# Kernel optimization log

Measured on AMD Instinct MI355X. Metric: run time of the kernel, lower is better.

The kernel has to match this reference:

```python
import jax, jax.numpy as jnp
import numpy as np

HEADS = 64
DIM_HEAD = 64
SCALE = DIM_HEAD ** -0.5
EPS = 1e-6


def setup_inputs() -> dict:
    key = jax.random.key(0)
    ks = jax.random.split(key, 6)
    b, s, dim = 2, 4096, 1024
    inner = HEADS * DIM_HEAD  # 4096
    std = 0.02
    return {
        "x": jax.random.normal(ks[0], (b, s, dim), dtype=jnp.float32),
        "Wq": jax.random.normal(ks[1], (dim, inner), dtype=jnp.float32) * std,
        "Wk": jax.random.normal(ks[2], (dim, inner), dtype=jnp.float32) * std,
        "Wv": jax.random.normal(ks[3], (dim, inner), dtype=jnp.float32) * std,
        "Wo": jax.random.normal(ks[4], (inner, dim), dtype=jnp.float32) * std,
        "bo": jnp.zeros((dim,), dtype=jnp.float32),
    }


def reference(x, Wq, Wk, Wv, Wo, bo):
    b, s, dim = x.shape
    h, dh = HEADS, DIM_HEAD
    # projections -> [b, s, h, dh]
    q = (x @ Wq).reshape(b, s, h, dh)
    k = (x @ Wk).reshape(b, s, h, dh)
    v = (x @ Wv).reshape(b, s, h, dh)
    # kernel feature map (relu) + scale on q
    q = jax.nn.relu(q) * SCALE
    k = jax.nn.relu(k)
    # NOTE: faithful to the source, these einsums contract over the HEAD axis
    # per token (i, j index heads; d indexes dim_head).
    kv = jnp.einsum('bsid,bsjd->bsdj', k, v)          # [b, s, dh, h]
    out = jnp.einsum('bsid,bsdj->bsij', q, kv)        # [b, s, h, h]
    q_norm = jnp.einsum('bsid,bsd->bsi', q, k.sum(axis=2))  # [b, s, h]
    out = out / (q_norm[..., None] + EPS)
    out = out.reshape(b, s, h * h)                    # h*h == h*dh since h == dh
    return out @ Wo + bo
```

## Files before the change

### kernel.cpp

```cpp
#include <hip/hip_runtime.h>
#include <hip/hip_bf16.h>
#include <cstdint>

#define M_TOK 8192
#define DIM   1024
#define INNER 4096
#define HEADS 64
#define DH    64
#define QSCALE 0.125f
#define EPS    1e-6f

typedef __hip_bfloat16 bf16;
typedef __bf16 bf16x8_t __attribute__((ext_vector_type(8)));
typedef float f32x4_t __attribute__((ext_vector_type(4)));

__device__ __forceinline__ float bfbits2f(unsigned short u) {
  return __uint_as_float(((unsigned)u) << 16);
}
__device__ __forceinline__ unsigned short f2bfbits(float f) {
  __hip_bfloat16 h = __float2bfloat16(f);
  unsigned short u;
  __builtin_memcpy(&u, &h, 2);
  return u;
}

__device__ __forceinline__ void load_lds16(const void* g, void* l) {
  __builtin_amdgcn_global_load_lds(
      (__attribute__((address_space(1))) void*)g,
      (__attribute__((address_space(3))) void*)l, 16, 0, 0);
}

__device__ __forceinline__ void asm_barrier() {
  asm volatile("s_barrier" ::: "memory");
}

__device__ __forceinline__ void swizzle_xy(int& bx, int& by) {
  const int gx = gridDim.x, gy = gridDim.y;
  const int id  = blockIdx.x + gx * blockIdx.y;
  const int per = gy >> 3;
  const int xcd = id & 7;
  const int s   = id >> 3;
  by = xcd * per + (s % per);
  bx = s / per;
}

__global__ __launch_bounds__(256) void castx_kernel(
    const float* __restrict__ x, unsigned short* __restrict__ xb, int n4)
{
  const int i = blockIdx.x * 256 + threadIdx.x;
  if (i < n4) {
    const float4 v = reinterpret_cast<const float4*>(x)[i];
    ushort4 o;
    o.x = f2bfbits(v.x); o.y = f2bfbits(v.y);
    o.z = f2bfbits(v.z); o.w = f2bfbits(v.w);
    reinterpret_cast<ushort4*>(xb)[i] = o;
  }
}

__global__ __launch_bounds__(256) void tcast_kernel(
    const float* __restrict__ W, unsigned short* __restrict__ Wt, int R, int C)
{
  __shared__ float tile[32][33];
  const int bx = blockIdx.x * 32;
  const int by = blockIdx.y * 32;
  const int tx = threadIdx.x & 31;
  const int ty = threadIdx.x >> 5;
#pragma unroll
  for (int k = 0; k < 4; ++k)
    tile[ty + k * 8][tx] = W[(size_t)(by + ty + k * 8) * C + bx + tx];
  __syncthreads();
#pragma unroll
  for (int k = 0; k < 4; ++k)
    Wt[(size_t)(bx + ty + k * 8) * R + by + tx] = f2bfbits(tile[tx][ty + k * 8]);
}

__global__ __launch_bounds__(256) void tcast_dual_kernel(
    const float* __restrict__ W0, const float* __restrict__ W1,
    unsigned short* __restrict__ Wt, int R, int C)
{
  __shared__ float tile[32][33];
  const float* W = blockIdx.z ? W1 : W0;
  unsigned short* dst = Wt + (size_t)blockIdx.z * R * C;
  const int bx = blockIdx.x * 32;
  const int by = blockIdx.y * 32;
  const int tx = threadIdx.x & 31;
  const int ty = threadIdx.x >> 5;
#pragma unroll
  for (int k = 0; k < 4; ++k)
    tile[ty + k * 8][tx] = W[(size_t)(by + ty + k * 8) * C + bx + tx];
  __syncthreads();
#pragma unroll
  for (int k = 0; k < 4; ++k)
    dst[(size_t)(bx + ty + k * 8) * R + by + tx] = f2bfbits(tile[tx][ty + k * 8]);
}

__device__ __forceinline__ void stage_half(
    const unsigned short* __restrict__ G, unsigned short* L,
    int rowbase, int k0, int K, int h, int tid)
{
#pragma unroll
  for (int j = 0; j < 2; ++j) {
    const int q  = h * 1024 + j * 512 + tid;
    const int r  = q >> 3;
    const int cg = (tid & 7) ^ (r & 7);
    load_lds16(&G[(size_t)(rowbase + r) * K + k0 + cg * 8], &L[q * 8]);
  }
}

template <int MODE, int DUAL>
__global__ __launch_bounds__(512, 2) void gemm256(
    const unsigned short* __restrict__ A,
    const unsigned short* __restrict__ Bt,
    unsigned short* __restrict__ C0,
    unsigned short* __restrict__ C1,
    int N, int K)
{
  __shared__ __align__(16) unsigned short As[2][256 * 64];
  __shared__ __align__(16) unsigned short Bs[2][256 * 64];

  int bxi, byi;
  swizzle_xy(bxi, byi);
  const int tid  = threadIdx.x;
  const int bm   = byi * 256;
  const int bn   = bxi * 256;
  const int lane = tid & 63;
  const int w    = tid >> 6;
  const int wm   = (w >> 2) * 128;
  const int wn   = (w & 3) * 64;
  const int quad = lane >> 4;
  const int l15  = lane & 15;

  f32x4_t acc[8][4];
#pragma unroll
  for (int mt = 0; mt < 8; ++mt)
#pragma unroll
    for (int nt = 0; nt < 4; ++nt) acc[mt][nt] = (f32x4_t){0.f, 0.f, 0.f, 0.f};

  const int NT = K >> 6;

  stage_half(A,  As[0], bm, 0,  K, 0, tid);
  stage_half(A,  As[0], bm, 0,  K, 1, tid);
  stage_half(Bt, Bs[0], bn, 0,  K, 0, tid);
  stage_half(Bt, Bs[0], bn, 0,  K, 1, tid);
  stage_half(A,  As[1], bm, 64, K, 0, tid);
  stage_half(A,  As[1], bm, 64, K, 1, tid);
  asm volatile("s_waitcnt vmcnt(4)" ::: "memory");
  asm_barrier();

  bf16x8_t af[8][2], bfr[4][2];

  for (int T = 0; T < NT; ++T) {
    const int c = T & 1;
    const unsigned short* Ac = As[c];
    const unsigned short* Bc = Bs[c];
    unsigned short* Bnx = Bs[c ^ 1];
    unsigned short* Anx = As[c];
    const int kB = (T + 1) * 64;
    const int kA = (T + 2) * 64;
    const bool pB = (T + 1 < NT);
    const bool pA = (T + 2 < NT);

#pragma unroll
    for (int mt = 0; mt < 4; ++mt) {
      const int r = wm + mt * 16 + l15;
#pragma unroll
      for (int kt = 0; kt < 2; ++kt) {
        const int s = (kt * 4 + quad) ^ (r & 7);
        af[mt][kt] = *reinterpret_cast<const bf16x8_t*>(&Ac[r * 64 + s * 8]);
      }
    }
#pragma unroll
    for (int nt = 0; nt < 2; ++nt) {
      const int r = wn + nt * 16 + l15;
#pragma unroll
      for (int kt = 0; kt < 2; ++kt) {
        const int s = (kt * 4 + quad) ^ (r & 7);
        bfr[nt][kt] = *reinterpret_cast<const bf16x8_t*>(&Bc[r * 64 + s * 8]);
      }
    }
    if (pB) stage_half(Bt, Bnx, bn, kB, K, 0, tid);
    asm_barrier();
    __builtin_amdgcn_s_setprio(1);
#pragma unroll
    for (int mt = 0; mt < 4; ++mt)
#pragma unroll
      for (int nt = 0; nt < 2; ++nt) {
        acc[mt][nt] = __builtin_amdgcn_mfma_f32_16x16x32_bf16(
            af[mt][0], bfr[nt][0], acc[mt][nt], 0, 0, 0);
        acc[mt][nt] = __builtin_amdgcn_mfma_f32_16x16x32_bf16(
            af[mt][1], bfr[nt][1], acc[mt][nt], 0, 0, 0);
      }
    __builtin_amdgcn_s_setprio(0);
    asm_barrier();

#pragma unroll
    for (int mt = 4; mt < 8; ++mt) {
      const int r = wm + mt * 16 + l15;
#pragma unroll
      for (int kt = 0; kt < 2; ++kt) {
        const int s = (kt * 4 + quad) ^ (r & 7);
        af[mt][kt] = *reinterpret_cast<const bf16x8_t*>(&Ac[r * 64 + s * 8]);
      }
    }
    if (pB) stage_half(Bt, Bnx, bn, kB, K, 1, tid);
    asm_barrier();
    __builtin_amdgcn_s_setprio(1);
#pragma unroll
    for (int mt = 4; mt < 8; ++mt)
#pragma unroll
      for (int nt = 0; nt < 2; ++nt) {
        acc[mt][nt] = __builtin_amdgcn_mfma_f32_16x16x32_bf16(
            af[mt][0], bfr[nt][0], acc[mt][nt], 0, 0, 0);
        acc[mt][nt] = __builtin_amdgcn_mfma_f32_16x16x32_bf16(
            af[mt][1], bfr[nt][1], acc[mt][nt], 0, 0, 0);
      }
    __builtin_amdgcn_s_setprio(0);
    asm_barrier();

#pragma unroll
    for (int nt = 2; nt < 4; ++nt) {
      const int r = wn + nt * 16 + l15;
#pragma unroll
      for (int kt = 0; kt < 2; ++kt) {
        const int s = (kt * 4 + quad) ^ (r & 7);
        bfr[nt][kt] = *reinterpret_cast<const bf16x8_t*>(&Bc[r * 64 + s * 8]);
      }
    }
    if (pA) stage_half(A, Anx, bm, kA, K, 0, tid);
    asm_barrier();
    __builtin_amdgcn_s_setprio(1);
#pragma unroll
    for (int mt = 0; mt < 4; ++mt)
#pragma unroll
      for (int nt = 2; nt < 4; ++nt) {
        acc[mt][nt] = __builtin_amdgcn_mfma_f32_16x16x32_bf16(
            af[mt][0], bfr[nt][0], acc[mt][nt], 0, 0, 0);
        acc[mt][nt] = __builtin_amdgcn_mfma_f32_16x16x32_bf16(
            af[mt][1], bfr[nt][1], acc[mt][nt], 0, 0, 0);
      }
    __builtin_amdgcn_s_setprio(0);
    asm_barrier();

    if (pA) stage_half(A, Anx, bm, kA, K, 1, tid);
    asm_barrier();
    __builtin_amdgcn_s_setprio(1);
#pragma unroll
    for (int mt = 4; mt < 8; ++mt)
#pragma unroll
      for (int nt = 2; nt < 4; ++nt) {
        acc[mt][nt] = __builtin_amdgcn_mfma_f32_16x16x32_bf16(
            af[mt][0], bfr[nt][0], acc[mt][nt], 0, 0, 0);
        acc[mt][nt] = __builtin_amdgcn_mfma_f32_16x16x32_bf16(
            af[mt][1], bfr[nt][1], acc[mt][nt], 0, 0, 0);
      }
    __builtin_amdgcn_s_setprio(0);
    if (T < NT - 2) {
      asm volatile("s_waitcnt vmcnt(4)" ::: "memory");
    } else {
      asm volatile("s_waitcnt vmcnt(0)" ::: "memory");
    }
    asm_barrier();
  }

  if (DUAL) {
    const bool isK = (bn < 4096);
    unsigned short* __restrict__ C = isK ? C0 : C1;
    const int bnc = bn & 4095;
#pragma unroll
    for (int mt = 0; mt < 8; ++mt)
#pragma unroll
      for (int i = 0; i < 4; ++i) {
        const size_t rowg = (size_t)(bm + wm + mt * 16 + quad * 4 + i);
#pragma unroll
        for (int nt = 0; nt < 4; ++nt) {
          float v = acc[mt][nt][i];
          if (isK) v = fmaxf(v, 0.f);
          C[rowg * 4096 + bnc + wn + nt * 16 + l15] = f2bfbits(v);
        }
      }
  } else {
#pragma unroll
    for (int mt = 0; mt < 8; ++mt)
#pragma unroll
      for (int i = 0; i < 4; ++i) {
        const size_t rowg = (size_t)(bm + wm + mt * 16 + quad * 4 + i);
#pragma unroll
        for (int nt = 0; nt < 4; ++nt) {
          float v = acc[mt][nt][i];
          if (MODE >= 1) v = fmaxf(v, 0.f);
          if (MODE == 2) v *= QSCALE;
          C0[rowg * (size_t)N + bn + wn + nt * 16 + l15] = f2bfbits(v);
        }
      }
  }
}

__global__ __launch_bounds__(256) void gemm_out_bf16(
    const unsigned short* __restrict__ A,
    const unsigned short* __restrict__ Bt,
    const float* __restrict__ bias,
    float* __restrict__ out, int M, int N, int K)
{
  __shared__ __align__(16) unsigned short As[128 * 64];
  __shared__ __align__(16) unsigned short Bs[64 * 64];

  int bxi, byi;
  swizzle_xy(bxi, byi);
  const int tid  = threadIdx.x;
  const int bm   = byi * 128;
  const int bn   = bxi * 64;
  const int lane = tid & 63;
  const int w    = tid >> 6;
  const int wm   = (w & 1) * 64;
  const int wn   = (w >> 1) * 32;
  const int quad = lane >> 4;
  const int l15  = lane & 15;

  f32x4_t acc[4][2];
#pragma unroll
  for (int mt = 0; mt < 4; ++mt)
#pragma unroll
    for (int nt = 0; nt < 2; ++nt) acc[mt][nt] = (f32x4_t){0.f, 0.f, 0.f, 0.f};

  int qa[4], ra[4], ca[4];
#pragma unroll
  for (int j = 0; j < 4; ++j) {
    qa[j] = tid + 256 * j;
    ra[j] = qa[j] >> 3;
    ca[j] = (qa[j] & 7) ^ (ra[j] & 7);
  }
  int qb[2], rb[2], cb[2];
#pragma unroll
  for (int j = 0; j < 2; ++j) {
    qb[j] = tid + 256 * j;
    rb[j] = qb[j] >> 3;
    cb[j] = (qb[j] & 7) ^ (rb[j] & 7);
  }

  for (int k0 = 0; k0 < K; k0 += 64) {
    __syncthreads();
#pragma unroll
    for (int j = 0; j < 4; ++j)
      load_lds16(&A[(size_t)(bm + ra[j]) * K + k0 + ca[j] * 8], &As[qa[j] * 8]);
#pragma unroll
    for (int j = 0; j < 2; ++j)
      load_lds16(&Bt[(size_t)(bn + rb[j]) * K + k0 + cb[j] * 8], &Bs[qb[j] * 8]);
    __syncthreads();

    bf16x8_t af[4][2], bfr[2][2];
#pragma unroll
    for (int mt = 0; mt < 4; ++mt) {
      const int r = wm + mt * 16 + l15;
#pragma unroll
      for (int kt = 0; kt < 2; ++kt) {
        const int slot = (kt * 4 + quad) ^ (r & 7);
        af[mt][kt] = *reinterpret_cast<const bf16x8_t*>(&As[r * 64 + slot * 8]);
      }
    }
#pragma unroll
    for (int nt = 0; nt < 2; ++nt) {
      const int r = wn + nt * 16 + l15;
#pragma unroll
      for (int kt = 0; kt < 2; ++kt) {
        const int slot = (kt * 4 + quad) ^ (r & 7);
        bfr[nt][kt] = *reinterpret_cast<const bf16x8_t*>(&Bs[r * 64 + slot * 8]);
      }
    }
#pragma unroll
    for (int mt = 0; mt < 4; ++mt)
#pragma unroll
      for (int nt = 0; nt < 2; ++nt) {
        acc[mt][nt] = __builtin_amdgcn_mfma_f32_16x16x32_bf16(
            af[mt][0], bfr[nt][0], acc[mt][nt], 0, 0, 0);
        acc[mt][nt] = __builtin_amdgcn_mfma_f32_16x16x32_bf16(
            af[mt][1], bfr[nt][1], acc[mt][nt], 0, 0, 0);
      }
  }

#pragma unroll
  for (int mt = 0; mt < 4; ++mt)
#pragma unroll
    for (int i = 0; i < 4; ++i) {
      const size_t rowg = (size_t)(bm + wm + mt * 16 + quad * 4 + i);
#pragma unroll
      for (int nt = 0; nt < 2; ++nt) {
        const int colg = bn + wn + nt * 16 + l15;
        out[rowg * N + colg] = acc[mt][nt][i] + bias[colg];
      }
    }
}

__global__ __launch_bounds__(256) void ksum_kernel(
    const unsigned short* __restrict__ Kb, float* __restrict__ ks)
{
  const int t = blockIdx.x * 4 + (threadIdx.x >> 6);
  const int j = threadIdx.x & 63;
  const uint4* row = reinterpret_cast<const uint4*>(Kb + (size_t)t * INNER);
  float s[8] = {0.f, 0.f, 0.f, 0.f, 0.f, 0.f, 0.f, 0.f};
#pragma unroll
  for (int m = 0; m < 8; ++m) {
    const uint4 u = row[j + 64 * m];
    s[0] += __uint_as_float((u.x & 0xFFFFu) << 16);
    s[1] += __uint_as_float(u.x & 0xFFFF0000u);
    s[2] += __uint_as_float((u.y & 0xFFFFu) << 16);
    s[3] += __uint_as_float(u.y & 0xFFFF0000u);
    s[4] += __uint_as_float((u.z & 0xFFFFu) << 16);
    s[5] += __uint_as_float(u.z & 0xFFFF0000u);
    s[6] += __uint_as_float((u.w & 0xFFFFu) << 16);
    s[7] += __uint_as_float(u.w & 0xFFFF0000u);
  }
#pragma unroll
  for (int off = 8; off < 64; off <<= 1)
#pragma unroll
    for (int e = 0; e < 8; ++e) s[e] += __shfl_xor(s[e], off, 64);
  if (j < 8) {
    float4* dst = reinterpret_cast<float4*>(ks + t * 64 + j * 8);
    float4 lo, hi;
    lo.x = s[0]; lo.y = s[1]; lo.z = s[2]; lo.w = s[3];
    hi.x = s[4]; hi.y = s[5]; hi.z = s[6]; hi.w = s[7];
    dst[0] = lo; dst[1] = hi;
  }
}

__global__ __launch_bounds__(256) void attn_mfma(
    const unsigned short* __restrict__ Qb, const unsigned short* __restrict__ Vb,
    const float* __restrict__ ksum, unsigned short* __restrict__ Ab)
{
  const int t    = blockIdx.x * 4 + (threadIdx.x >> 6);
  const int lane = threadIdx.x & 63;
  const int l15  = lane & 15;
  const int quad = lane >> 4;
  const size_t base = (size_t)t * INNER;

  union VU { bf16x8_t v; unsigned short u[8]; };

  float ksv[2][8];
#pragma unroll
  for (int kt = 0; kt < 2; ++kt) {
    const float4* p = reinterpret_cast<const float4*>(ksum + t * 64 + kt * 32 + quad * 8);
    const float4 a = p[0], b = p[1];
    ksv[kt][0] = a.x; ksv[kt][1] = a.y; ksv[kt][2] = a.z; ksv[kt][3] = a.w;
    ksv[kt][4] = b.x; ksv[kt][5] = b.y; ksv[kt][6] = b.z; ksv[kt][7] = b.w;
  }

  bf16x8_t vs[4][2];
#pragma unroll
  for (int nt = 0; nt < 4; ++nt)
#pragma unroll
    for (int kt = 0; kt < 2; ++kt) {
      VU vr, vo;
      vr.v = *reinterpret_cast<const bf16x8_t*>(
          Vb + base + (size_t)(nt * 16 + l15) * 64 + kt * 32 + quad * 8);
#pragma unroll
      for (int j = 0; j < 8; ++j)
        vo.u[j] = f2bfbits(bfbits2f(vr.u[j]) * ksv[kt][j]);
      vs[nt][kt] = vo.v;
    }

  bf16x8_t qf[4][2];
  float qn[4] = {0.f, 0.f, 0.f, 0.f};
#pragma unroll
  for (int mt = 0; mt < 4; ++mt)
#pragma unroll
    for (int kt = 0; kt < 2; ++kt) {
      VU qr;
      qr.v = *reinterpret_cast<const bf16x8_t*>(
          Qb + base + (size_t)(mt * 16 + l15) * 64 + kt * 32 + quad * 8);
      qf[mt][kt] = qr.v;
#pragma unroll
      for (int j = 0; j < 8; ++j)
        qn[mt] += bfbits2f(qr.u[j]) * ksv[kt][j];
    }
#pragma unroll
  for (int mt = 0; mt < 4; ++mt) {
    qn[mt] += __shfl_xor(qn[mt], 16, 64);
    qn[mt] += __shfl_xor(qn[mt], 32, 64);
  }

  f32x4_t acc[4][4];
#pragma unroll
  for (int mt = 0; mt < 4; ++mt)
#pragma unroll
    for (int nt = 0; nt < 4; ++nt) acc[mt][nt] = (f32x4_t){0.f, 0.f, 0.f, 0.f};

#pragma unroll
  for (int mt = 0; mt < 4; ++mt)
#pragma unroll
    for (int nt = 0; nt < 4; ++nt) {
      acc[mt][nt] = __builtin_amdgcn_mfma_f32_16x16x32_bf16(
          qf[mt][0], vs[nt][0], acc[mt][nt], 0, 0, 0);
      acc[mt][nt] = __builtin_amdgcn_mfma_f32_16x16x32_bf16(
          qf[mt][1], vs[nt][1], acc[mt][nt], 0, 0, 0);
    }

#pragma unroll
  for (int mt = 0; mt < 4; ++mt)
#pragma unroll
    for (int i = 0; i < 4; ++i) {
      const float inv = 1.f / (__shfl(qn[mt], quad * 4 + i, 64) + EPS);
      const size_t roff = base + (size_t)(mt * 16 + quad * 4 + i) * 64;
#pragma unroll
      for (int nt = 0; nt < 4; ++nt)
        Ab[roff + nt * 16 + l15] = f2bfbits(acc[mt][nt][i] * inv);
    }
}

extern "C" void kernel_launch(void* const* d_in, const int* in_sizes, int n_in,
                              void* d_out, int out_size, void* d_ws, size_t ws_size,
                              hipStream_t stream)
{
  const float* x  = (const float*)d_in[0];
  const float* Wq = (const float*)d_in[1];
  const float* Wk = (const float*)d_in[2];
  const float* Wv = (const float*)d_in[3];
  const float* Wo = (const float*)d_in[4];
  const float* bo = (const float*)d_in[5];
  float* out = (float*)d_out;

  uint8_t* ws = (uint8_t*)d_ws;
  const size_t HALF = (size_t)M_TOK * INNER * sizeof(bf16);
  unsigned short* KQA = (unsigned short*)ws;
  unsigned short* Vb  = (unsigned short*)(ws + HALF);
  float* ks           = (float*)(ws + 2 * HALF);

  unsigned short* Xb   = (unsigned short*)d_out;
  unsigned short* WtKV = (unsigned short*)((uint8_t*)d_out + (16u << 20));
  unsigned short* WqT  = WtKV;
  unsigned short* Wot  = Vb;

  const dim3 blk(256);
  const dim3 blk512(512);

  castx_kernel<<<dim3(M_TOK * DIM / 4 / 256), blk, 0, stream>>>(
      x, Xb, M_TOK * DIM / 4);

  tcast_dual_kernel<<<dim3(INNER / 32, DIM / 32, 2), blk, 0, stream>>>(
      Wk, Wv, WtKV, DIM, INNER);

  gemm256<0, 1><<<dim3(2 * INNER / 256, M_TOK / 256), blk512, 0, stream>>>(
      Xb, WtKV, KQA, Vb, 2 * INNER, DIM);

  ksum_kernel<<<dim3(M_TOK / 4), blk, 0, stream>>>(KQA, ks);

  tcast_kernel<<<dim3(INNER / 32, DIM / 32), blk, 0, stream>>>(
      Wq, WqT, DIM, INNER);

  gemm256<2, 0><<<dim3(INNER / 256, M_TOK / 256), blk512, 0, stream>>>(
      Xb, WqT, KQA, nullptr, INNER, DIM);

  attn_mfma<<<dim3(M_TOK / 4), blk, 0, stream>>>(KQA, Vb, ks, KQA);

  tcast_kernel<<<dim3(DIM / 32, INNER / 32), blk, 0, stream>>>(
      Wo, Wot, INNER, DIM);

  gemm_out_bf16<<<dim3(DIM / 64, M_TOK / 128), blk, 0, stream>>>(
      KQA, Wot, bo, out, M_TOK, DIM, INNER);
}
```

Measured before the change: 487.1 us.

## Software-pipeline LDS fragment reads with MFMA and drop intra-iteration barriers

Restructures the GEMM main loop so LDS fragment reads for the next sub-block are issued before the current MFMA group, gated by explicit lgkmcnt waits and sched_barriers instead of workgroup s_barriers. The first A/B fragments of the next K-tile are prefetched right after the end-of-iteration barrier. The aim is to hide LDS read latency behind matrix-core work and remove three barriers per iteration. It relies on the existing double-buffer plan staying race-free without those barriers, since the async global-to-LDS writes now overlap other waves' reads more loosely.

```diff
diff --git a/kernel.cpp b/kernel.cpp
--- a/kernel.cpp
+++ b/kernel.cpp
@@ -33,6 +33,10 @@
 __device__ __forceinline__ void asm_barrier() {
   asm volatile("s_barrier" ::: "memory");
 }
+
+#define LGKM_SB(N) do { \
+    asm volatile("s_waitcnt lgkmcnt(" #N ")" ::: "memory"); \
+    __builtin_amdgcn_sched_barrier(0); } while (0)
 
 __device__ __forceinline__ void swizzle_xy(int& bx, int& by) {
   const int gx = gridDim.x, gy = gridDim.y;
@@ -105,6 +109,53 @@
     const int cg = (tid & 7) ^ (r & 7);
     load_lds16(&G[(size_t)(rowbase + r) * K + k0 + cg * 8], &L[q * 8]);
   }
+}
+
+__device__ __forceinline__ void read_af4(
+    const unsigned short* __restrict__ Ac, bf16x8_t (&af)[8][2],
+    int m0, int wm, int l15, int quad)
+{
+#pragma unroll
+  for (int mt = 0; mt < 4; ++mt) {
+    const int r = wm + (m0 + mt) * 16 + l15;
+#pragma unroll
+    for (int kt = 0; kt < 2; ++kt) {
+      const int s = (kt * 4 + quad) ^ (r & 7);
+      af[m0 + mt][kt] = *reinterpret_cast<const bf16x8_t*>(&Ac[r * 64 + s * 8]);
+    }
+  }
+}
+
+__device__ __forceinline__ void read_bf2(
+    const unsigned short* __restrict__ Bc, bf16x8_t (&bfr)[4][2],
+    int n0, int wn, int l15, int quad)
+{
+#pragma unroll
+  for (int nt = 0; nt < 2; ++nt) {
+    const int r = wn + (n0 + nt) * 16 + l15;
+#pragma unroll
+    for (int kt = 0; kt < 2; ++kt) {
+      const int s = (kt * 4 + quad) ^ (r & 7);
+      bfr[n0 + nt][kt] = *reinterpret_cast<const bf16x8_t*>(&Bc[r * 64 + s * 8]);
+    }
+  }
+}
+
+__device__ __forceinline__ void mfma_quad(
+    f32x4_t (&acc)[8][4], const bf16x8_t (&af)[8][2],
+    const bf16x8_t (&bfr)[4][2], int m0, int n0)
+{
+  __builtin_amdgcn_s_setprio(1);
+#pragma unroll
+  for (int mt = m0; mt < m0 + 4; ++mt)
+#pragma unroll
+    for (int nt = n0; nt < n0 + 2; ++nt) {
+      acc[mt][nt] = __builtin_amdgcn_mfma_f32_16x16x32_bf16(
+          af[mt][0], bfr[nt][0], acc[mt][nt], 0, 0, 0);
+      acc[mt][nt] = __builtin_amdgcn_mfma_f32_16x16x32_bf16(
+          af[mt][1], bfr[nt][1], acc[mt][nt], 0, 0, 0);
+    }
+  __builtin_amdgcn_s_setprio(0);
 }
 
 template <int MODE, int DUAL>
@@ -138,6 +189,8 @@
 
   const int NT = K >> 6;
 
+  bf16x8_t af[8][2], bfr[4][2];
+
   stage_half(A,  As[0], bm, 0,  K, 0, tid);
   stage_half(A,  As[0], bm, 0,  K, 1, tid);
   stage_half(Bt, Bs[0], bn, 0,  K, 0, tid);
@@ -146,8 +199,9 @@
   stage_half(A,  As[1], bm, 64, K, 1, tid);
   asm volatile("s_waitcnt vmcnt(4)" ::: "memory");
   asm_barrier();
-
-  bf16x8_t af[8][2], bfr[4][2];
+  __builtin_amdgcn_sched_barrier(0);
+  read_af4(As[0], af, 0, wm, l15, quad);
+  read_bf2(Bs[0], bfr, 0, wn, l15, quad);
 
   for (int T = 0; T < NT; ++T) {
     const int c = T & 1;
@@ -160,106 +214,33 @@
     const bool pB = (T + 1 < NT);
     const bool pA = (T + 2 < NT);
 
-#pragma unroll
-    for (int mt = 0; mt < 4; ++mt) {
-      const int r = wm + mt * 16 + l15;
-#pragma unroll
-      for (int kt = 0; kt < 2; ++kt) {
-        const int s = (kt * 4 + quad) ^ (r & 7);
-        af[mt][kt] = *reinterpret_cast<const bf16x8_t*>(&Ac[r * 64 + s * 8]);
-      }
-    }
-#pragma unroll
-    for (int nt = 0; nt < 2; ++nt) {
-      const int r = wn + nt * 16 + l15;
-#pragma unroll
-      for (int kt = 0; kt < 2; ++kt) {
-        const int s = (kt * 4 + quad) ^ (r & 7);
-        bfr[nt][kt] = *reinterpret_cast<const bf16x8_t*>(&Bc[r * 64 + s * 8]);
-      }
-    }
+    read_af4(Ac, af, 4, wm, l15, quad);
+    LGKM_SB(8);
+    mfma_quad(acc, af, bfr, 0, 0);
+
+    read_bf2(Bc, bfr, 2, wn, l15, quad);
     if (pB) stage_half(Bt, Bnx, bn, kB, K, 0, tid);
-    asm_barrier();
-    __builtin_amdgcn_s_setprio(1);
-#pragma unroll
-    for (int mt = 0; mt < 4; ++mt)
-#pragma unroll
-      for (int nt = 0; nt < 2; ++nt) {
-        acc[mt][nt] = __builtin_amdgcn_mfma_f32_16x16x32_bf16(
-            af[mt][0], bfr[nt][0], acc[mt][nt], 0, 0, 0);
-        acc[mt][nt] = __builtin_amdgcn_mfma_f32_16x16x32_bf16(
-            af[mt][1], bfr[nt][1], acc[mt][nt], 0, 0, 0);
-      }
-    __builtin_amdgcn_s_setprio(0);
-    asm_barrier();
-
-#pragma unroll
-    for (int mt = 4; mt < 8; ++mt) {
-      const int r = wm + mt * 16 + l15;
-#pragma unroll
-      for (int kt = 0; kt < 2; ++kt) {
-        const int s = (kt * 4 + quad) ^ (r & 7);
-        af[mt][kt] = *reinterpret_cast<const bf16x8_t*>(&Ac[r * 64 + s * 8]);
-      }
-    }
+    LGKM_SB(4);
+    mfma_quad(acc, af, bfr, 4, 0);
+
     if (pB) stage_half(Bt, Bnx, bn, kB, K, 1, tid);
-    asm_barrier();
-    __builtin_amdgcn_s_setprio(1);
-#pragma unroll
-    for (int mt = 4; mt < 8; ++mt)
-#pragma unroll
-      for (int nt = 0; nt < 2; ++nt) {
-        acc[mt][nt] = __builtin_amdgcn_mfma_f32_16x16x32_bf16(
-            af[mt][0], bfr[nt][0], acc[mt][nt], 0, 0, 0);
-        acc[mt][nt] = __builtin_amdgcn_mfma_f32_16x16x32_bf16(
-            af[mt][1], bfr[nt][1], acc[mt][nt], 0, 0, 0);
-      }
-    __builtin_amdgcn_s_setprio(0);
-    asm_barrier();
-
-#pragma unroll
-    for (int nt = 2; nt < 4; ++nt) {
-      const int r = wn + nt * 16 + l15;
-#pragma unroll
-      for (int kt = 0; kt < 2; ++kt) {
-        const int s = (kt * 4 + quad) ^ (r & 7);
-        bfr[nt][kt] = *reinterpret_cast<const bf16x8_t*>(&Bc[r * 64 + s * 8]);
-      }
-    }
     if (pA) stage_half(A, Anx, bm, kA, K, 0, tid);
-    asm_barrier();
-    __builtin_amdgcn_s_setprio(1);
-#pragma unroll
-    for (int mt = 0; mt < 4; ++mt)
-#pragma unroll
-      for (int nt = 2; nt < 4; ++nt) {
-        acc[mt][nt] = __builtin_amdgcn_mfma_f32_16x16x32_bf16(
-            af[mt][0], bfr[nt][0], acc[mt][nt], 0, 0, 0);
-        acc[mt][nt] = __builtin_amdgcn_mfma_f32_16x16x32_bf16(
-            af[mt][1], bfr[nt][1], acc[mt][nt], 0, 0, 0);
-      }
-    __builtin_amdgcn_s_setprio(0);
-    asm_barrier();
+    LGKM_SB(0);
+    mfma_quad(acc, af, bfr, 0, 2);
 
     if (pA) stage_half(A, Anx, bm, kA, K, 1, tid);
-    asm_barrier();
-    __builtin_amdgcn_s_setprio(1);
-#pragma unroll
-    for (int mt = 4; mt < 8; ++mt)
-#pragma unroll
-      for (int nt = 2; nt < 4; ++nt) {
-        acc[mt][nt] = __builtin_amdgcn_mfma_f32_16x16x32_bf16(
-            af[mt][0], bfr[nt][0], acc[mt][nt], 0, 0, 0);
-        acc[mt][nt] = __builtin_amdgcn_mfma_f32_16x16x32_bf16(
-            af[mt][1], bfr[nt][1], acc[mt][nt], 0, 0, 0);
-      }
-    __builtin_amdgcn_s_setprio(0);
+    mfma_quad(acc, af, bfr, 4, 2);
     if (T < NT - 2) {
       asm volatile("s_waitcnt vmcnt(4)" ::: "memory");
     } else {
       asm volatile("s_waitcnt vmcnt(0)" ::: "memory");
     }
     asm_barrier();
+    __builtin_amdgcn_sched_barrier(0);
+    if (T + 1 < NT) {
+      read_af4(As[c ^ 1], af, 0, wm, l15, quad);
+      read_bf2(Bs[c ^ 1], bfr, 0, wn, l15, quad);
+    }
   }
 
   if (DUAL) {
```

Result: faster. 465.1 us (-4.5%).
